# Kernel tuning notes

Measured on AMD Instinct MI355X. Metric: run time of the kernel, lower is better.

## Reference

```python
import jax, jax.numpy as jnp
import numpy as np

B, C, N = 8, 256, 4096

def setup_inputs() -> dict:
    key = jax.random.key(0)
    k1, k2, k3 = jax.random.split(key, 3)
    pts_feat = jax.random.normal(k1, (B, C, N), dtype=jnp.float32)
    # Conv1d(channels, channels, 1, bias=False) weight is [C_out, C_in, 1] -> store as [C_out, C_in]
    scale = 1.0 / np.sqrt(C)
    Wq = jax.random.uniform(k2, (C, C), dtype=jnp.float32, minval=-scale, maxval=scale)
    Wk = jax.random.uniform(k3, (C, C), dtype=jnp.float32, minval=-scale, maxval=scale)
    return {"pts_feat": pts_feat, "Wq": Wq, "Wk": Wk}

def reference(pts_feat, Wq, Wk):
    # 1x1 conv == channel-wise matmul. x_q: [B, N, C], x_k: [B, C, N]
    x_q = jnp.einsum('bcn,dc->bnd', pts_feat, Wq)
    x_k = jnp.einsum('bcn,dc->bdn', pts_feat, Wk)
    logits = jnp.einsum('bnc,bcm->bnm', x_q, x_k)          # [B, N, N]
    attn = jax.nn.softmax(logits, axis=-1)
    attn = attn / (1e-8 + attn.sum(axis=-1, keepdims=True))
    # torch.einsum('bnn,bnc->bnc', attn, feat) takes the DIAGONAL of attn
    # and scales each point's raw feature vector by it (no contraction).
    diag = jnp.diagonal(attn, axis1=1, axis2=2)            # [B, N]
    x_attn = pts_feat * diag[:, None, :]                   # [B, C, N]
    return x_attn
```

## Files before the change

### kernel.cpp

```cpp
#include <hip/hip_runtime.h>
#include <hip/hip_bf16.h>
#include <cstdint>

#define B_ 8
#define C_ 256
#define N_ 4096

typedef __bf16 bf16;
typedef __bf16 bf16x8 __attribute__((ext_vector_type(8)));
typedef float f32x4 __attribute__((ext_vector_type(4)));
typedef unsigned int u32;

__device__ __forceinline__ void async_ld16(const void* g, void* l) {
  __builtin_amdgcn_global_load_lds(
      (const __attribute__((address_space(1))) void*)g,
      (__attribute__((address_space(3))) void*)l, 16, 0, 0);
}

__device__ __forceinline__ float bh2f(unsigned short u) {
  union { u32 i; float f; } x; x.i = ((u32)u) << 16; return x.f;
}
__device__ __forceinline__ unsigned short f2bh(float f) {
  union { float f; u32 i; } x; x.f = f;
  u32 i = x.i + 0x7fffu + ((x.i >> 16) & 1u);
  return (unsigned short)(i >> 16);
}

__device__ __forceinline__ bool wave_sniff_fp32(const unsigned short* p) {
  int l = threadIdx.x & 63;
  unsigned short u = p[2 * l];
  int e = (u >> 7) & 0xff;
  unsigned long long m = __ballot(e >= 112 && e <= 142);
  return __popcll(m) < 32;
}

__global__ __launch_bounds__(256) void k_pre(const void* __restrict__ Wqv,
                                             const void* __restrict__ Wkv,
                                             const void* __restrict__ Fv,
                                             unsigned short* __restrict__ Mt,
                                             unsigned short* __restrict__ Ft) {
  __shared__ float wkcol[C_];
  __shared__ unsigned short tile[64 * 66];
  int bid = blockIdx.x;
  int t = threadIdx.x;
  if (bid < 256) {
    bool fq = wave_sniff_fp32((const unsigned short*)Wqv);
    bool fk = wave_sniff_fp32((const unsigned short*)Wkv);
    int d = bid, c = t;
    if (fk)
      wkcol[c] = ((const float*)Wkv)[c * C_ + d];
    else
      wkcol[c] = bh2f(((const unsigned short*)Wkv)[c * C_ + d]);
    __syncthreads();
    float acc = 0.f;
    if (fq) {
      for (int e0 = 0; e0 < C_; e0 += 16) {
        float wq[16];
#pragma unroll
        for (int j = 0; j < 16; ++j) wq[j] = ((const float*)Wqv)[(e0 + j) * C_ + c];
#pragma unroll
        for (int j = 0; j < 16; ++j) acc += wkcol[e0 + j] * wq[j];
      }
    } else {
      for (int e0 = 0; e0 < C_; e0 += 16) {
        float wq[16];
#pragma unroll
        for (int j = 0; j < 16; ++j) wq[j] = bh2f(((const unsigned short*)Wqv)[(e0 + j) * C_ + c]);
#pragma unroll
        for (int j = 0; j < 16; ++j) acc += wkcol[e0 + j] * wq[j];
      }
    }
    Mt[(size_t)d * C_ + c] = f2bh(acc);
    return;
  }
  bool f32 = wave_sniff_fp32((const unsigned short*)Fv);
  int id = bid - 256;
  int n0 = (id & 63) * 64, c0 = ((id >> 6) & 3) * 64, b = id >> 8;
#pragma unroll
  for (int p = 0; p < 2; ++p) {
    int c = (t >> 3) + 32 * p;
    int n = (t & 7) * 8;
    size_t off = (size_t)(b * C_ + c0 + c) * N_ + n0 + n;
    unsigned short vals[8];
    if (f32) {
      const float* src = (const float*)Fv + off;
      float4 v0 = *(const float4*)(src);
      float4 v1 = *(const float4*)(src + 4);
      vals[0] = f2bh(v0.x); vals[1] = f2bh(v0.y); vals[2] = f2bh(v0.z); vals[3] = f2bh(v0.w);
      vals[4] = f2bh(v1.x); vals[5] = f2bh(v1.y); vals[6] = f2bh(v1.z); vals[7] = f2bh(v1.w);
    } else {
      uint4 v = *(const uint4*)((const unsigned short*)Fv + off);
      vals[0] = (unsigned short)(v.x & 0xffffu); vals[1] = (unsigned short)(v.x >> 16);
      vals[2] = (unsigned short)(v.y & 0xffffu); vals[3] = (unsigned short)(v.y >> 16);
      vals[4] = (unsigned short)(v.z & 0xffffu); vals[5] = (unsigned short)(v.z >> 16);
      vals[6] = (unsigned short)(v.w & 0xffffu); vals[7] = (unsigned short)(v.w >> 16);
    }
#pragma unroll
    for (int s = 0; s < 8; ++s) tile[c * 66 + n + s] = vals[s];
  }
  __syncthreads();
#pragma unroll
  for (int p = 0; p < 2; ++p) {
    int n = (t >> 3) + 32 * p;
    int c8 = (t & 7) * 8;
    u32 o[4];
#pragma unroll
    for (int k = 0; k < 4; ++k) {
      unsigned short lo = tile[(c8 + 2 * k) * 66 + n];
      unsigned short hi = tile[(c8 + 2 * k + 1) * 66 + n];
      o[k] = ((u32)hi << 16) | lo;
    }
    uint4 ov; ov.x = o[0]; ov.y = o[1]; ov.z = o[2]; ov.w = o[3];
    *(uint4*)(Ft + ((size_t)(b * N_ + n0 + n) * C_ + c0 + c8)) = ov;
  }
}

__global__ __launch_bounds__(256, 4) void k_proj(const bf16* __restrict__ Ft,
                                                 const bf16* __restrict__ Mt,
                                                 bf16* __restrict__ G) {
  __shared__ bf16 As[8 * 64 * 32];
  int n0 = blockIdx.x * 64;
  int b = blockIdx.y;
  int d0 = blockIdx.z * 128;
  int t = threadIdx.x, w = t >> 6, l = t & 63;
  int lr = l & 15, lq = l >> 4;
  int wn = w * 32;
  const size_t fbase = (size_t)b * N_ * C_;

  int srow = t >> 2;
  int schunk = ((t & 3) ^ ((t >> 3) & 3)) * 8;
#pragma unroll
  for (int kc = 0; kc < 8; ++kc)
    async_ld16(Ft + fbase + (size_t)(n0 + srow) * C_ + kc * 32 + schunk,
               As + kc * 2048 + t * 8);

  bf16x8 bb[2][8];
#pragma unroll
  for (int j = 0; j < 2; ++j)
#pragma unroll
    for (int kc = 0; kc < 8; ++kc)
      bb[j][kc] = *(const bf16x8*)(Mt + (size_t)(d0 + wn + 16 * j + lr) * C_ + kc * 32 + lq * 8);

  __syncthreads();
  int rchunk = (lq ^ ((lr >> 1) & 3)) * 8;
  f32x4 acc[4][2] = {};
#pragma unroll
  for (int kc = 0; kc < 8; ++kc) {
#pragma unroll
    for (int i = 0; i < 4; ++i) {
      bf16x8 a = *(const bf16x8*)(As + kc * 2048 + (16 * i + lr) * 32 + rchunk);
#pragma unroll
      for (int j = 0; j < 2; ++j)
        acc[i][j] = __builtin_amdgcn_mfma_f32_16x16x32_bf16(a, bb[j][kc], acc[i][j], 0, 0, 0);
    }
  }
  __syncthreads();
  unsigned short* Cs = (unsigned short*)As;
#pragma unroll
  for (int i = 0; i < 4; ++i)
#pragma unroll
    for (int j = 0; j < 2; ++j)
#pragma unroll
      for (int r = 0; r < 4; ++r)
        Cs[(16 * i + lq * 4 + r) * 136 + wn + 16 * j + lr] = f2bh(acc[i][j][r]);
  __syncthreads();
#pragma unroll
  for (int p = 0; p < 4; ++p) {
    int idx = p * 256 + t;
    int row = idx >> 4, c8 = idx & 15;
    uint4 v = *(const uint4*)(Cs + row * 136 + c8 * 8);
    *(uint4*)(G + fbase + (size_t)(n0 + row) * C_ + d0 + c8 * 8) = v;
  }
}

__global__ __launch_bounds__(256, 4) void k_attn(const bf16* __restrict__ G,
                                                 const bf16* __restrict__ Ft,
                                                 float* __restrict__ snn,
                                                 float* __restrict__ lsum) {
  __shared__ bf16 Ks[2][32 * 256];
  int bid = blockIdx.x;
  int b = bid & 7, q = (bid >> 3) & 3, ntile = bid >> 5;
  int n0 = ntile * 128;
  int t = threadIdx.x, w = t >> 6, l = t & 63;
  int lr = l & 15, lq = l >> 4;
  int wrow = w * 32;
  const size_t gbase = (size_t)b * N_ * C_;

  bf16x8 a[2][8];
#pragma unroll
  for (int i = 0; i < 2; ++i)
#pragma unroll
    for (int kc = 0; kc < 8; ++kc)
      a[i][kc] = *(const bf16x8*)(G + gbase + (size_t)(n0 + wrow + 16 * i + lr) * C_ + kc * 32 + lq * 8);

  float part[8];
#pragma unroll
  for (int s = 0; s < 8; ++s) part[s] = 0.f;

  int m_base = q * 1024;
  bool has_diag = (q == (ntile >> 3));
  int dbase = (ntile & 7) * 4;

  int soff[4];
#pragma unroll
  for (int p = 0; p < 4; ++p) {
    int flat = p * 256 + t;
    int kc = flat >> 7;
    int r = (flat >> 2) & 31;
    int col8 = flat & 3;
    soff[p] = r * C_ + kc * 32 + ((col8 ^ ((r >> 1) & 3)) * 8);
  }
  int rchunk = (lq ^ ((lr >> 1) & 3)) * 8;

#pragma unroll
  for (int p = 0; p < 4; ++p)
    async_ld16(Ft + gbase + (size_t)m_base * C_ + soff[p],
               (bf16*)Ks + (p * 256 + t) * 8);
  asm volatile("s_waitcnt vmcnt(0)" ::: "memory");
  __builtin_amdgcn_s_barrier();

  for (int it = 0; it < 32; ++it) {
    int cur = it & 1;
    if (it < 31) {
      int m0 = m_base + (it + 1) * 32;
#pragma unroll
      for (int p = 0; p < 4; ++p)
        async_ld16(Ft + gbase + (size_t)m0 * C_ + soff[p],
                   (bf16*)Ks + (cur ^ 1) * 8192 + (p * 256 + t) * 8);
    }
    const bf16* ks = (const bf16*)Ks + cur * 8192;
    f32x4 acc[2][2] = {};
#pragma unroll
    for (int kc = 0; kc < 8; ++kc) {
      bf16x8 b0 = *(const bf16x8*)(ks + kc * 1024 + lr * 32 + rchunk);
      bf16x8 b1 = *(const bf16x8*)(ks + kc * 1024 + (16 + lr) * 32 + rchunk);
      acc[0][0] = __builtin_amdgcn_mfma_f32_16x16x32_bf16(a[0][kc], b0, acc[0][0], 0, 0, 0);
      acc[1][0] = __builtin_amdgcn_mfma_f32_16x16x32_bf16(a[1][kc], b0, acc[1][0], 0, 0, 0);
      acc[0][1] = __builtin_amdgcn_mfma_f32_16x16x32_bf16(a[0][kc], b1, acc[0][1], 0, 0, 0);
      acc[1][1] = __builtin_amdgcn_mfma_f32_16x16x32_bf16(a[1][kc], b1, acc[1][1], 0, 0, 0);
    }
    bool dit = has_diag && ((it >> 2) == (ntile & 7));
#pragma unroll
    for (int i = 0; i < 2; ++i)
#pragma unroll
      for (int j = 0; j < 2; ++j)
#pragma unroll
        for (int r = 0; r < 4; ++r) {
          float e = __expf(acc[i][j][r]);
          part[i * 4 + r] += e;
          if (dit) {
            int rloc = wrow + 16 * i + lq * 4 + r;
            int cloc = 16 * j + lr;
            if ((it - dbase) * 32 + cloc == rloc) snn[b * N_ + n0 + rloc] = e;
          }
        }
    if (it < 31) {
      asm volatile("s_waitcnt vmcnt(0)" ::: "memory");
      __builtin_amdgcn_s_barrier();
    }
  }

#pragma unroll
  for (int s = 0; s < 8; ++s) {
    float v = part[s];
    v += __shfl_xor(v, 1);
    v += __shfl_xor(v, 2);
    v += __shfl_xor(v, 4);
    v += __shfl_xor(v, 8);
    part[s] = v;
  }
  if (lr == 0) {
#pragma unroll
    for (int i = 0; i < 2; ++i)
#pragma unroll
      for (int r = 0; r < 4; ++r)
        lsum[((size_t)q * B_ + b) * N_ + n0 + wrow + 16 * i + lq * 4 + r] = part[i * 4 + r];
  }
}

__global__ __launch_bounds__(256) void k_scale(const void* __restrict__ Fv,
                                               const float* __restrict__ snn,
                                               const float* __restrict__ lsum,
                                               void* __restrict__ Outv) {
  bool f32 = wave_sniff_fp32((const unsigned short*)Fv);
  int g = blockIdx.x * 256 + threadIdx.x;
  size_t base = (size_t)g * 8;
  int n = (int)(base & (N_ - 1));
  int b = (int)(base >> 20);
  float4 s0 = *(const float4*)(snn + (size_t)b * N_ + n);
  float4 s1 = *(const float4*)(snn + (size_t)b * N_ + n + 4);
  float ls[8];
#pragma unroll
  for (int k = 0; k < 8; ++k) ls[k] = 0.f;
#pragma unroll
  for (int p = 0; p < 4; ++p) {
    float4 l0 = *(const float4*)(lsum + ((size_t)p * B_ + b) * N_ + n);
    float4 l1 = *(const float4*)(lsum + ((size_t)p * B_ + b) * N_ + n + 4);
    ls[0] += l0.x; ls[1] += l0.y; ls[2] += l0.z; ls[3] += l0.w;
    ls[4] += l1.x; ls[5] += l1.y; ls[6] += l1.z; ls[7] += l1.w;
  }
  const float c1 = 1.0f + 1e-8f;
  float dd[8];
  dd[0] = s0.x / (ls[0] * c1); dd[1] = s0.y / (ls[1] * c1);
  dd[2] = s0.z / (ls[2] * c1); dd[3] = s0.w / (ls[3] * c1);
  dd[4] = s1.x / (ls[4] * c1); dd[5] = s1.y / (ls[5] * c1);
  dd[6] = s1.z / (ls[6] * c1); dd[7] = s1.w / (ls[7] * c1);
  if (f32) {
    const float* F = (const float*)Fv + base;
    float* O = (float*)Outv + base;
    float4 a0 = *(const float4*)(F);
    float4 a1 = *(const float4*)(F + 4);
    float4 o0, o1;
    o0.x = a0.x * dd[0]; o0.y = a0.y * dd[1]; o0.z = a0.z * dd[2]; o0.w = a0.w * dd[3];
    o1.x = a1.x * dd[4]; o1.y = a1.y * dd[5]; o1.z = a1.z * dd[6]; o1.w = a1.w * dd[7];
    *(float4*)(O) = o0;
    *(float4*)(O + 4) = o1;
  } else {
    uint4 v = *(const uint4*)((const unsigned short*)Fv + base);
    u32 vv[4] = {v.x, v.y, v.z, v.w};
    u32 o[4];
#pragma unroll
    for (int k = 0; k < 4; ++k) {
      float lo = bh2f((unsigned short)(vv[k] & 0xffffu)) * dd[2 * k];
      float hi = bh2f((unsigned short)(vv[k] >> 16)) * dd[2 * k + 1];
      o[k] = ((u32)f2bh(hi) << 16) | f2bh(lo);
    }
    uint4 ov; ov.x = o[0]; ov.y = o[1]; ov.z = o[2]; ov.w = o[3];
    *(uint4*)((unsigned short*)Outv + base) = ov;
  }
}

extern "C" void kernel_launch(void* const* d_in, const int* in_sizes, int n_in,
                              void* d_out, int out_size, void* d_ws, size_t ws_size,
                              hipStream_t stream) {
  (void)in_sizes; (void)n_in; (void)out_size; (void)ws_size;
  const void* F = d_in[0];
  const void* Wq = d_in[1];
  const void* Wk = d_in[2];
  char* ws = (char*)d_ws;
  bf16* Ft = (bf16*)(ws);
  bf16* G = (bf16*)(ws + (16u << 20));
  char* tail = ws + (32u << 20);
  float* snn = (float*)(tail);
  float* lsum = (float*)(tail + 131072);
  bf16* Mt = (bf16*)(tail + 131072 + 524288);

  k_pre<<<256 + 2048, 256, 0, stream>>>(Wq, Wk, F, (unsigned short*)Mt, (unsigned short*)Ft);
  k_proj<<<dim3(N_ / 64, B_, 2), 256, 0, stream>>>(Ft, Mt, G);
  k_attn<<<1024, 256, 0, stream>>>(G, Ft, snn, lsum);
  k_scale<<<(B_ * C_ * N_ / 8) / 256, 256, 0, stream>>>(F, snn, lsum, d_out);
}
```

Before: 177.0 us.

## Deepen K-tile pipeline to 4-stage ring of 16-row tiles with prefetch distance two

Replaces the double-buffered 32-row K tile loop with a 4-slot ring of 16-row tiles, issuing loads two tiles ahead and waiting with partial vmcnt counts instead of draining all loads each iteration. This is meant to hide global-to-LDS latency better and remove the full vmcnt(0) stall per step. It also raises wave priority around the MFMA block. The trade-off is twice as many iterations and barriers, with half the MFMA work per barrier, so synchronisation overhead per unit of compute goes up. LDS usage is unchanged.

```diff
diff --git a/kernel.cpp b/kernel.cpp
--- a/kernel.cpp
+++ b/kernel.cpp
@@ -177,7 +177,7 @@
                                                  const bf16* __restrict__ Ft,
                                                  float* __restrict__ snn,
                                                  float* __restrict__ lsum) {
-  __shared__ bf16 Ks[2][32 * 256];
+  __shared__ bf16 Ks[4][16 * 256];
   int bid = blockIdx.x;
   int b = bid & 7, q = (bid >> 3) & 3, ntile = bid >> 5;
   int n0 = ntile * 128;
@@ -199,65 +199,66 @@
 
   int m_base = q * 1024;
   bool has_diag = (q == (ntile >> 3));
-  int dbase = (ntile & 7) * 4;
-
-  int soff[4];
-#pragma unroll
-  for (int p = 0; p < 4; ++p) {
+  int dbase = (ntile & 7) * 8;
+
+  int soff[2];
+#pragma unroll
+  for (int p = 0; p < 2; ++p) {
     int flat = p * 256 + t;
-    int kc = flat >> 7;
-    int r = (flat >> 2) & 31;
+    int kc = flat >> 6;
+    int r = (flat >> 2) & 15;
     int col8 = flat & 3;
     soff[p] = r * C_ + kc * 32 + ((col8 ^ ((r >> 1) & 3)) * 8);
   }
   int rchunk = (lq ^ ((lr >> 1) & 3)) * 8;
 
 #pragma unroll
-  for (int p = 0; p < 4; ++p)
+  for (int p = 0; p < 2; ++p)
     async_ld16(Ft + gbase + (size_t)m_base * C_ + soff[p],
                (bf16*)Ks + (p * 256 + t) * 8);
-  asm volatile("s_waitcnt vmcnt(0)" ::: "memory");
-  __builtin_amdgcn_s_barrier();
-
-  for (int it = 0; it < 32; ++it) {
-    int cur = it & 1;
-    if (it < 31) {
-      int m0 = m_base + (it + 1) * 32;
-#pragma unroll
-      for (int p = 0; p < 4; ++p)
-        async_ld16(Ft + gbase + (size_t)m0 * C_ + soff[p],
-                   (bf16*)Ks + (cur ^ 1) * 8192 + (p * 256 + t) * 8);
-    }
-    const bf16* ks = (const bf16*)Ks + cur * 8192;
-    f32x4 acc[2][2] = {};
+#pragma unroll
+  for (int p = 0; p < 2; ++p)
+    async_ld16(Ft + gbase + (size_t)(m_base + 16) * C_ + soff[p],
+               (bf16*)Ks + 4096 + (p * 256 + t) * 8);
+
+  for (int it = 0; it < 64; ++it) {
+    if (it <= 61) {
+      int m0 = m_base + (it + 2) * 16;
+      bf16* dst = (bf16*)Ks + ((it + 2) & 3) * 4096;
+#pragma unroll
+      for (int p = 0; p < 2; ++p)
+        async_ld16(Ft + gbase + (size_t)m0 * C_ + soff[p], dst + (p * 256 + t) * 8);
+      asm volatile("s_waitcnt vmcnt(4)" ::: "memory");
+    } else if (it == 62) {
+      asm volatile("s_waitcnt vmcnt(2)" ::: "memory");
+    } else {
+      asm volatile("s_waitcnt vmcnt(0)" ::: "memory");
+    }
+    __builtin_amdgcn_s_barrier();
+
+    const bf16* ks = (const bf16*)Ks + (it & 3) * 4096;
+    f32x4 acc[2] = {};
+    __builtin_amdgcn_s_setprio(1);
 #pragma unroll
     for (int kc = 0; kc < 8; ++kc) {
-      bf16x8 b0 = *(const bf16x8*)(ks + kc * 1024 + lr * 32 + rchunk);
-      bf16x8 b1 = *(const bf16x8*)(ks + kc * 1024 + (16 + lr) * 32 + rchunk);
-      acc[0][0] = __builtin_amdgcn_mfma_f32_16x16x32_bf16(a[0][kc], b0, acc[0][0], 0, 0, 0);
-      acc[1][0] = __builtin_amdgcn_mfma_f32_16x16x32_bf16(a[1][kc], b0, acc[1][0], 0, 0, 0);
-      acc[0][1] = __builtin_amdgcn_mfma_f32_16x16x32_bf16(a[0][kc], b1, acc[0][1], 0, 0, 0);
-      acc[1][1] = __builtin_amdgcn_mfma_f32_16x16x32_bf16(a[1][kc], b1, acc[1][1], 0, 0, 0);
-    }
-    bool dit = has_diag && ((it >> 2) == (ntile & 7));
+      bf16x8 b0 = *(const bf16x8*)(ks + kc * 512 + lr * 32 + rchunk);
+      acc[0] = __builtin_amdgcn_mfma_f32_16x16x32_bf16(a[0][kc], b0, acc[0], 0, 0, 0);
+      acc[1] = __builtin_amdgcn_mfma_f32_16x16x32_bf16(a[1][kc], b0, acc[1], 0, 0, 0);
+    }
+    __builtin_amdgcn_s_setprio(0);
+
+    bool dit = has_diag && ((it >> 3) == (ntile & 7));
 #pragma unroll
     for (int i = 0; i < 2; ++i)
 #pragma unroll
-      for (int j = 0; j < 2; ++j)
-#pragma unroll
-        for (int r = 0; r < 4; ++r) {
-          float e = __expf(acc[i][j][r]);
-          part[i * 4 + r] += e;
-          if (dit) {
-            int rloc = wrow + 16 * i + lq * 4 + r;
-            int cloc = 16 * j + lr;
-            if ((it - dbase) * 32 + cloc == rloc) snn[b * N_ + n0 + rloc] = e;
-          }
+      for (int r = 0; r < 4; ++r) {
+        float e = __expf(acc[i][r]);
+        part[i * 4 + r] += e;
+        if (dit) {
+          int rloc = wrow + 16 * i + lq * 4 + r;
+          if ((it - dbase) * 16 + lr == rloc) snn[b * N_ + n0 + rloc] = e;
         }
-    if (it < 31) {
-      asm volatile("s_waitcnt vmcnt(0)" ::: "memory");
-      __builtin_amdgcn_s_barrier();
-    }
+      }
   }
 
 #pragma unroll
```

Measured after the change: 184.0 us. +3.9%, slower.

## Fold log2e into M for exp2 softmax, restructure scale kernel per tile

Applied to the files above, without the earlier changes.

The weight product M is pre-scaled by log2(e), so the attention kernel can call the native exp2 instruction instead of __expf. The scale kernel now has each block cover one batch and a 64-point tile across all channels. Its 64 diagonal factors are computed once per block into LDS, replacing the per-thread lsum/snn reloads and divisions repeated for every channel. The trade-off is fewer blocks (512) each doing more work per thread, plus bf16 rounding now applied to the scaled M values.

```diff
diff --git a/kernel.cpp b/kernel.cpp
--- a/kernel.cpp
+++ b/kernel.cpp
@@ -70,7 +70,7 @@
         for (int j = 0; j < 16; ++j) acc += wkcol[e0 + j] * wq[j];
       }
     }
-    Mt[(size_t)d * C_ + c] = f2bh(acc);
+    Mt[(size_t)d * C_ + c] = f2bh(acc * 1.44269504f);
     return;
   }
   bool f32 = wave_sniff_fp32((const unsigned short*)Fv);
@@ -246,7 +246,7 @@
       for (int j = 0; j < 2; ++j)
 #pragma unroll
         for (int r = 0; r < 4; ++r) {
-          float e = __expf(acc[i][j][r]);
+          float e = __builtin_amdgcn_exp2f(acc[i][j][r]);
           part[i * 4 + r] += e;
           if (dit) {
             int rloc = wrow + 16 * i + lq * 4 + r;
@@ -282,51 +282,55 @@
                                                const float* __restrict__ snn,
                                                const float* __restrict__ lsum,
                                                void* __restrict__ Outv) {
+  __shared__ __align__(16) float dd_lds[64];
   bool f32 = wave_sniff_fp32((const unsigned short*)Fv);
-  int g = blockIdx.x * 256 + threadIdx.x;
-  size_t base = (size_t)g * 8;
-  int n = (int)(base & (N_ - 1));
-  int b = (int)(base >> 20);
-  float4 s0 = *(const float4*)(snn + (size_t)b * N_ + n);
-  float4 s1 = *(const float4*)(snn + (size_t)b * N_ + n + 4);
-  float ls[8];
-#pragma unroll
-  for (int k = 0; k < 8; ++k) ls[k] = 0.f;
-#pragma unroll
-  for (int p = 0; p < 4; ++p) {
-    float4 l0 = *(const float4*)(lsum + ((size_t)p * B_ + b) * N_ + n);
-    float4 l1 = *(const float4*)(lsum + ((size_t)p * B_ + b) * N_ + n + 4);
-    ls[0] += l0.x; ls[1] += l0.y; ls[2] += l0.z; ls[3] += l0.w;
-    ls[4] += l1.x; ls[5] += l1.y; ls[6] += l1.z; ls[7] += l1.w;
-  }
-  const float c1 = 1.0f + 1e-8f;
-  float dd[8];
-  dd[0] = s0.x / (ls[0] * c1); dd[1] = s0.y / (ls[1] * c1);
-  dd[2] = s0.z / (ls[2] * c1); dd[3] = s0.w / (ls[3] * c1);
-  dd[4] = s1.x / (ls[4] * c1); dd[5] = s1.y / (ls[5] * c1);
-  dd[6] = s1.z / (ls[6] * c1); dd[7] = s1.w / (ls[7] * c1);
+  int bid = blockIdx.x;
+  int b = bid >> 6, n0 = (bid & 63) * 64;
+  int t = threadIdx.x;
+  if (t < 64) {
+    int n = n0 + t;
+    float s = snn[(size_t)b * N_ + n];
+    float ls = 0.f;
+#pragma unroll
+    for (int p = 0; p < 4; ++p) ls += lsum[((size_t)p * B_ + b) * N_ + n];
+    dd_lds[t] = s / (ls * (1.0f + 1e-8f));
+  }
+  __syncthreads();
+  const size_t fb = (size_t)b * C_ * N_;
   if (f32) {
-    const float* F = (const float*)Fv + base;
-    float* O = (float*)Outv + base;
-    float4 a0 = *(const float4*)(F);
-    float4 a1 = *(const float4*)(F + 4);
-    float4 o0, o1;
-    o0.x = a0.x * dd[0]; o0.y = a0.y * dd[1]; o0.z = a0.z * dd[2]; o0.w = a0.w * dd[3];
-    o1.x = a1.x * dd[4]; o1.y = a1.y * dd[5]; o1.z = a1.z * dd[6]; o1.w = a1.w * dd[7];
-    *(float4*)(O) = o0;
-    *(float4*)(O + 4) = o1;
+    const float* F = (const float*)Fv;
+    float* O = (float*)Outv;
+#pragma unroll
+    for (int p = 0; p < 16; ++p) {
+      int idx = p * 256 + t;
+      int c = idx >> 4, ch = idx & 15;
+      size_t off = fb + (size_t)c * N_ + n0 + ch * 4;
+      float4 v = *(const float4*)(F + off);
+      float4 d = *(const float4*)(&dd_lds[ch * 4]);
+      float4 o;
+      o.x = v.x * d.x; o.y = v.y * d.y; o.z = v.z * d.z; o.w = v.w * d.w;
+      *(float4*)(O + off) = o;
+    }
   } else {
-    uint4 v = *(const uint4*)((const unsigned short*)Fv + base);
-    u32 vv[4] = {v.x, v.y, v.z, v.w};
-    u32 o[4];
-#pragma unroll
-    for (int k = 0; k < 4; ++k) {
-      float lo = bh2f((unsigned short)(vv[k] & 0xffffu)) * dd[2 * k];
-      float hi = bh2f((unsigned short)(vv[k] >> 16)) * dd[2 * k + 1];
-      o[k] = ((u32)f2bh(hi) << 16) | f2bh(lo);
-    }
-    uint4 ov; ov.x = o[0]; ov.y = o[1]; ov.z = o[2]; ov.w = o[3];
-    *(uint4*)((unsigned short*)Outv + base) = ov;
+    const unsigned short* F = (const unsigned short*)Fv;
+    unsigned short* O = (unsigned short*)Outv;
+#pragma unroll
+    for (int p = 0; p < 8; ++p) {
+      int idx = p * 256 + t;
+      int c = idx >> 3, ch = idx & 7;
+      size_t off = fb + (size_t)c * N_ + n0 + ch * 8;
+      uint4 v = *(const uint4*)(F + off);
+      u32 vv[4] = {v.x, v.y, v.z, v.w};
+      u32 o[4];
+#pragma unroll
+      for (int k = 0; k < 4; ++k) {
+        float lo = bh2f((unsigned short)(vv[k] & 0xffffu)) * dd_lds[ch * 8 + 2 * k];
+        float hi = bh2f((unsigned short)(vv[k] >> 16)) * dd_lds[ch * 8 + 2 * k + 1];
+        o[k] = ((u32)f2bh(hi) << 16) | f2bh(lo);
+      }
+      uint4 ov; ov.x = o[0]; ov.y = o[1]; ov.z = o[2]; ov.w = o[3];
+      *(uint4*)(O + off) = ov;
+    }
   }
 }
 
@@ -348,5 +352,5 @@
   k_pre<<<256 + 2048, 256, 0, stream>>>(Wq, Wk, F, (unsigned short*)Mt, (unsigned short*)Ft);
   k_proj<<<dim3(N_ / 64, B_, 2), 256, 0, stream>>>(Ft, Mt, G);
   k_attn<<<1024, 256, 0, stream>>>(G, Ft, snn, lsum);
-  k_scale<<<(B_ * C_ * N_ / 8) / 256, 256, 0, stream>>>(F, snn, lsum, d_out);
-}
+  k_scale<<<512, 256, 0, stream>>>(F, snn, lsum, d_out);
+}
```

Measured after the change: 169.8 us. -4.1%, faster.
